# Optimization experiments

Measured on AMD Instinct MI355X. Metric: run time of the kernel, lower is better.

## Reference

```python
import jax, jax.numpy as jnp
import numpy as np

NEG_INF = -9e15
ALPHA = 2.0  # LeakyReLU negative slope from init (alpha=2)


def setup_inputs() -> dict:
    key = jax.random.key(0)
    k1, k2, k3, k4 = jax.random.split(key, 4)
    B, N, Fin, Fout = 8, 2048, 256, 128
    x = jax.random.normal(k1, (B, N, Fin), dtype=jnp.float32)
    adj = jax.random.randint(k2, (B, N, N), 0, 2, dtype=jnp.int32)
    # xavier_uniform with gain=1.414
    def xavier(k, shape, gain=1.414):
        fan_in, fan_out = shape[0], shape[1]
        bound = gain * np.sqrt(6.0 / (fan_in + fan_out))
        return jax.random.uniform(k, shape, jnp.float32, -bound, bound)
    W = xavier(k3, (Fin, Fout))
    a = xavier(k4, (2 * Fout, 1))
    return {"x": x, "adj": adj, "W": W, "a": a}


def reference(x, adj, W, a):
    # Wh: [B, N, Fout]
    Wh = jnp.matmul(x, W)
    Fout = W.shape[1]
    a1 = a[:Fout, 0]   # [Fout]
    a2 = a[Fout:, 0]   # [Fout]
    f1 = jnp.einsum('bnf,f->bn', Wh, a1)  # [B, N]
    f2 = jnp.einsum('bnf,f->bn', Wh, a2)  # [B, N]
    e = f1[:, :, None] + f2[:, None, :]   # [B, N, N]
    e = jnp.where(e >= 0, e, ALPHA * e)   # leaky relu, slope 2
    e = jnp.where(adj > 0, e, NEG_INF)
    attention = jax.nn.softmax(e, axis=2)
    # dropout: eval mode (no-op)
    h_prime = jnp.matmul(attention, Wh)   # [B, N, Fout]
    # concat=True -> elu
    return jnp.where(h_prime > 0, h_prime, jnp.expm1(h_prime))
```

## Files before the change

### kernel.cpp

```cpp
#include <hip/hip_runtime.h>
#include <hip/hip_bf16.h>
#include <math.h>

constexpr int B_   = 8;
constexpr int N_   = 2048;
constexpr int FIN  = 256;
constexpr int FOUT = 128;

constexpr int CH  = 512;
constexpr int NCH = N_ / CH;
constexpr int PR  = CH + 8;
constexpr int XR  = FIN + 8;
constexpr int TR  = 40;

typedef __attribute__((ext_vector_type(8))) short bf16x8;
typedef __attribute__((ext_vector_type(4))) float f32x4;
typedef __attribute__((ext_vector_type(4))) int   i32x4;

static __device__ __forceinline__ unsigned short f2bf(float f) {
    __hip_bfloat16 h = __float2bfloat16(f);
    return *reinterpret_cast<unsigned short*>(&h);
}
static __device__ __forceinline__ i32x4 ntload4(const int* p) {
    return __builtin_nontemporal_load((const i32x4*)p);
}

__global__ __launch_bounds__(256) void k0_wt(const float* __restrict__ W,
                                             unsigned short* __restrict__ Wt) {
    const int n = blockIdx.x;
    const int k = threadIdx.x;
    Wt[n * FIN + k] = f2bf(W[k * FOUT + n]);
}

__global__ __launch_bounds__(256) void ka_wh(const float* __restrict__ x,
                                             const unsigned short* __restrict__ Wt,
                                             const float* __restrict__ a,
                                             unsigned short* __restrict__ WhT,
                                             float* __restrict__ f1,
                                             float* __restrict__ f2) {
    __shared__ unsigned short xs[32 * XR];
    __shared__ float as[2 * FOUT];
    __shared__ float fred[2][4][32];

    const int tid = threadIdx.x;
    const int j0  = blockIdx.x * 32;
    const int b   = j0 >> 11;
    const int jb  = j0 & (N_ - 1);

    if (tid < 2 * FOUT) as[tid] = a[tid];
    {
        const float4* xsrc = (const float4*)(x + (size_t)j0 * FIN);
#pragma unroll
        for (int t = 0; t < 8; ++t) {
            const int idx = tid + t * 256;
            float4 v = xsrc[idx];
            const int row = idx >> 6, c4 = idx & 63;
            ushort4 u;
            u.x = f2bf(v.x); u.y = f2bf(v.y); u.z = f2bf(v.z); u.w = f2bf(v.w);
            *(ushort4*)&xs[row * XR + c4 * 4] = u;
        }
    }
    __syncthreads();

    const int wave = tid >> 6, lane = tid & 63;
    const int quad = lane >> 4, l16 = lane & 15;

    f32x4 acc[2][2];
#pragma unroll
    for (int aa = 0; aa < 2; ++aa)
#pragma unroll
        for (int nn = 0; nn < 2; ++nn) acc[aa][nn] = {0.f, 0.f, 0.f, 0.f};

    const unsigned short* wtA0 = Wt + (size_t)(32 * wave + l16) * FIN;
    const unsigned short* wtA1 = wtA0 + 16 * FIN;
#pragma unroll
    for (int ks = 0; ks < FIN / 32; ++ks) {
        const int kof = ks * 32 + quad * 8;
        bf16x8 af0 = *(const bf16x8*)&wtA0[kof];
        bf16x8 af1 = *(const bf16x8*)&wtA1[kof];
        bf16x8 bf0 = *(const bf16x8*)&xs[l16 * XR + kof];
        bf16x8 bf1 = *(const bf16x8*)&xs[(16 + l16) * XR + kof];
        acc[0][0] = __builtin_amdgcn_mfma_f32_16x16x32_bf16(af0, bf0, acc[0][0], 0, 0, 0);
        acc[0][1] = __builtin_amdgcn_mfma_f32_16x16x32_bf16(af0, bf1, acc[0][1], 0, 0, 0);
        acc[1][0] = __builtin_amdgcn_mfma_f32_16x16x32_bf16(af1, bf0, acc[1][0], 0, 0, 0);
        acc[1][1] = __builtin_amdgcn_mfma_f32_16x16x32_bf16(af1, bf1, acc[1][1], 0, 0, 0);
    }
    __syncthreads();

    unsigned short* T = xs;
    float pf[2][2] = {{0.f, 0.f}, {0.f, 0.f}};
#pragma unroll
    for (int aa = 0; aa < 2; ++aa)
#pragma unroll
        for (int nn = 0; nn < 2; ++nn)
#pragma unroll
            for (int r = 0; r < 4; ++r) {
                const int d = 32 * wave + 16 * aa + 4 * quad + r;
                const float v = acc[aa][nn][r];
                T[d * TR + nn * 16 + l16] = f2bf(v);
                pf[0][nn] += v * as[d];
                pf[1][nn] += v * as[FOUT + d];
            }
#pragma unroll
    for (int ff = 0; ff < 2; ++ff)
#pragma unroll
        for (int nn = 0; nn < 2; ++nn) {
            float v = pf[ff][nn];
            v += __shfl_xor(v, 16);
            v += __shfl_xor(v, 32);
            pf[ff][nn] = v;
        }
    if (quad == 0) {
#pragma unroll
        for (int ff = 0; ff < 2; ++ff)
#pragma unroll
            for (int nn = 0; nn < 2; ++nn)
                fred[ff][wave][nn * 16 + l16] = pf[ff][nn];
    }
    __syncthreads();

    unsigned short* dstW = WhT + (size_t)b * FOUT * N_;
#pragma unroll
    for (int it = 0; it < 2; ++it) {
        const int idx = it * 256 + tid;
        const int d = idx >> 2, q = idx & 3;
        bf16x8 v = *(const bf16x8*)&T[d * TR + q * 8];
        *(bf16x8*)&dstW[(size_t)d * N_ + jb + q * 8] = v;
    }
    if (tid < 64) {
        const int ff = tid >> 5, j32 = tid & 31;
        const float s = fred[ff][0][j32] + fred[ff][1][j32] +
                        fred[ff][2][j32] + fred[ff][3][j32];
        (ff ? f2 : f1)[(size_t)b * N_ + jb + j32] = s;
    }
}

static __device__ __forceinline__ void kb_phaseA(
    const int c, const int lane, const int wave, const int i0,
    const int* __restrict__ adjB, const float4* __restrict__ f2b4,
    const float* __restrict__ f1r, float* __restrict__ s_run,
    unsigned short* __restrict__ pb)
{
    const float4 fv0 = f2b4[c * (CH / 4) + lane];
    const float4 fv1 = f2b4[c * (CH / 4) + 64 + lane];
#pragma unroll
    for (int rr = 0; rr < 4; ++rr) {
        const int ti = wave * 4 + rr;
        const int i  = i0 + ti;
        const int* arow = adjB + (size_t)i * N_ + c * CH;
        const i32x4 av0 = ntload4(arow + 4 * lane);
        const i32x4 av1 = ntload4(arow + 256 + 4 * lane);
        const float f1i = f1r[rr];

        float e[8];
        e[0] = f1i + fv0.x; e[1] = f1i + fv0.y; e[2] = f1i + fv0.z; e[3] = f1i + fv0.w;
        e[4] = f1i + fv1.x; e[5] = f1i + fv1.y; e[6] = f1i + fv1.z; e[7] = f1i + fv1.w;
#pragma unroll
        for (int q = 0; q < 8; ++q) e[q] = (e[q] >= 0.f) ? e[q] : 2.f * e[q];

        float pv[8];
        pv[0] = (av0.x > 0) ? __expf(e[0]) : 0.f;
        pv[1] = (av0.y > 0) ? __expf(e[1]) : 0.f;
        pv[2] = (av0.z > 0) ? __expf(e[2]) : 0.f;
        pv[3] = (av0.w > 0) ? __expf(e[3]) : 0.f;
        pv[4] = (av1.x > 0) ? __expf(e[4]) : 0.f;
        pv[5] = (av1.y > 0) ? __expf(e[5]) : 0.f;
        pv[6] = (av1.z > 0) ? __expf(e[6]) : 0.f;
        pv[7] = (av1.w > 0) ? __expf(e[7]) : 0.f;

        s_run[rr] += ((pv[0] + pv[1]) + (pv[2] + pv[3])) +
                     ((pv[4] + pv[5]) + (pv[6] + pv[7]));

        ushort4 u0, u1;
        u0.x = f2bf(pv[0]); u0.y = f2bf(pv[1]); u0.z = f2bf(pv[2]); u0.w = f2bf(pv[3]);
        u1.x = f2bf(pv[4]); u1.y = f2bf(pv[5]); u1.z = f2bf(pv[6]); u1.w = f2bf(pv[7]);
        *(ushort4*)&pb[ti * PR + 4 * lane]       = u0;
        *(ushort4*)&pb[ti * PR + 256 + 4 * lane] = u1;
    }
}

__global__ __launch_bounds__(256) void kb_attn(const int* __restrict__ adj,
                                               const unsigned short* __restrict__ WhT,
                                               const float* __restrict__ f1,
                                               const float* __restrict__ f2,
                                               float* __restrict__ out) {
    __shared__ unsigned short p[2][16 * PR];
    __shared__ float rsum[16];

    const int tid  = threadIdx.x;
    const int b    = blockIdx.x & 7;
    const int i0   = (blockIdx.x >> 3) * 16;
    const int wave = tid >> 6, lane = tid & 63;
    const int quad = lane >> 4, l16 = lane & 15;

    const float4* f2b4 = (const float4*)(f2 + (size_t)b * N_);
    const int*    adjB = adj + (size_t)b * N_ * N_;

    float f1r[4], s_run[4];
#pragma unroll
    for (int rr = 0; rr < 4; ++rr) {
        f1r[rr]   = f1[(size_t)b * N_ + i0 + wave * 4 + rr];
        s_run[rr] = 0.f;
    }

    f32x4 acc0 = {0.f, 0.f, 0.f, 0.f}, acc1 = {0.f, 0.f, 0.f, 0.f};
    const int n0 = wave * 32;
    const unsigned short* wB0 = WhT + (size_t)b * FOUT * N_ + (size_t)(n0 + l16) * N_;
    const unsigned short* wB1 = wB0 + (size_t)16 * N_;

    kb_phaseA(0, lane, wave, i0, adjB, f2b4, f1r, s_run, &p[0][0]);
    __syncthreads();

    for (int c = 0; c < NCH; ++c) {
        if (c + 1 < NCH) {
            kb_phaseA(c + 1, lane, wave, i0, adjB, f2b4, f1r, s_run,
                      &p[(c + 1) & 1][0]);
        } else {
#pragma unroll
            for (int rr = 0; rr < 4; ++rr) {
                float s = s_run[rr];
#pragma unroll
                for (int o = 32; o; o >>= 1) s += __shfl_xor(s, o);
                if (lane == 0) rsum[wave * 4 + rr] = s;
            }
        }

        const unsigned short* pA = &p[c & 1][l16 * PR];
        const int kbase = c * CH;
#pragma unroll
        for (int ks = 0; ks < CH / 32; ++ks) {
            const int kof = ks * 32 + quad * 8;
            bf16x8 afr = *(const bf16x8*)&pA[kof];
            bf16x8 b0  = *(const bf16x8*)&wB0[kbase + kof];
            bf16x8 b1  = *(const bf16x8*)&wB1[kbase + kof];
            acc0 = __builtin_amdgcn_mfma_f32_16x16x32_bf16(afr, b0, acc0, 0, 0, 0);
            acc1 = __builtin_amdgcn_mfma_f32_16x16x32_bf16(afr, b1, acc1, 0, 0, 0);
        }
        __syncthreads();
    }

#pragma unroll
    for (int r = 0; r < 4; ++r) {
        const int m = quad * 4 + r;
        const float inv = 1.f / rsum[m];
        float v0 = acc0[r] * inv;
        float v1 = acc1[r] * inv;
        v0 = (v0 > 0.f) ? v0 : expm1f(v0);
        v1 = (v1 > 0.f) ? v1 : expm1f(v1);
        const size_t base = ((size_t)b * N_ + i0 + m) * FOUT + n0;
        out[base + l16]      = v0;
        out[base + 16 + l16] = v1;
    }
}

extern "C" void kernel_launch(void* const* d_in, const int* in_sizes, int n_in,
                              void* d_out, int out_size, void* d_ws, size_t ws_size,
                              hipStream_t stream) {
    const float* x   = (const float*)d_in[0];
    const int*   adj = (const int*)d_in[1];
    const float* W   = (const float*)d_in[2];
    const float* a   = (const float*)d_in[3];
    float* out = (float*)d_out;

    unsigned short* WhT = (unsigned short*)d_ws;
    unsigned short* Wt  = WhT + (size_t)B_ * FOUT * N_;
    float* f1 = (float*)(Wt + (size_t)FOUT * FIN);
    float* f2 = f1 + (size_t)B_ * N_;

    hipLaunchKernelGGL(k0_wt, dim3(FOUT), dim3(FIN), 0, stream, W, Wt);
    hipLaunchKernelGGL(ka_wh, dim3(B_ * N_ / 32), dim3(256), 0, stream,
                       x, Wt, a, WhT, f1, f2);
    hipLaunchKernelGGL(kb_attn, dim3(B_ * N_ / 16), dim3(256), 0, stream,
                       adj, WhT, f1, f2, out);
}
```

Baseline: 258.3 us.

## Use 8 waves per attention block and software-pipeline adj loads around MFMA

Result: no change. 260.2 us (+0.7%).

```diff
diff --git a/kernel.cpp b/kernel.cpp
--- a/kernel.cpp
+++ b/kernel.cpp
@@ -135,55 +135,11 @@
     }
 }
 
-static __device__ __forceinline__ void kb_phaseA(
-    const int c, const int lane, const int wave, const int i0,
-    const int* __restrict__ adjB, const float4* __restrict__ f2b4,
-    const float* __restrict__ f1r, float* __restrict__ s_run,
-    unsigned short* __restrict__ pb)
-{
-    const float4 fv0 = f2b4[c * (CH / 4) + lane];
-    const float4 fv1 = f2b4[c * (CH / 4) + 64 + lane];
-#pragma unroll
-    for (int rr = 0; rr < 4; ++rr) {
-        const int ti = wave * 4 + rr;
-        const int i  = i0 + ti;
-        const int* arow = adjB + (size_t)i * N_ + c * CH;
-        const i32x4 av0 = ntload4(arow + 4 * lane);
-        const i32x4 av1 = ntload4(arow + 256 + 4 * lane);
-        const float f1i = f1r[rr];
-
-        float e[8];
-        e[0] = f1i + fv0.x; e[1] = f1i + fv0.y; e[2] = f1i + fv0.z; e[3] = f1i + fv0.w;
-        e[4] = f1i + fv1.x; e[5] = f1i + fv1.y; e[6] = f1i + fv1.z; e[7] = f1i + fv1.w;
-#pragma unroll
-        for (int q = 0; q < 8; ++q) e[q] = (e[q] >= 0.f) ? e[q] : 2.f * e[q];
-
-        float pv[8];
-        pv[0] = (av0.x > 0) ? __expf(e[0]) : 0.f;
-        pv[1] = (av0.y > 0) ? __expf(e[1]) : 0.f;
-        pv[2] = (av0.z > 0) ? __expf(e[2]) : 0.f;
-        pv[3] = (av0.w > 0) ? __expf(e[3]) : 0.f;
-        pv[4] = (av1.x > 0) ? __expf(e[4]) : 0.f;
-        pv[5] = (av1.y > 0) ? __expf(e[5]) : 0.f;
-        pv[6] = (av1.z > 0) ? __expf(e[6]) : 0.f;
-        pv[7] = (av1.w > 0) ? __expf(e[7]) : 0.f;
-
-        s_run[rr] += ((pv[0] + pv[1]) + (pv[2] + pv[3])) +
-                     ((pv[4] + pv[5]) + (pv[6] + pv[7]));
-
-        ushort4 u0, u1;
-        u0.x = f2bf(pv[0]); u0.y = f2bf(pv[1]); u0.z = f2bf(pv[2]); u0.w = f2bf(pv[3]);
-        u1.x = f2bf(pv[4]); u1.y = f2bf(pv[5]); u1.z = f2bf(pv[6]); u1.w = f2bf(pv[7]);
-        *(ushort4*)&pb[ti * PR + 4 * lane]       = u0;
-        *(ushort4*)&pb[ti * PR + 256 + 4 * lane] = u1;
-    }
-}
-
-__global__ __launch_bounds__(256) void kb_attn(const int* __restrict__ adj,
-                                               const unsigned short* __restrict__ WhT,
-                                               const float* __restrict__ f1,
-                                               const float* __restrict__ f2,
-                                               float* __restrict__ out) {
+__global__ __launch_bounds__(512, 4) void kb_attn(const int* __restrict__ adj,
+                                                  const unsigned short* __restrict__ WhT,
+                                                  const float* __restrict__ f1,
+                                                  const float* __restrict__ f2,
+                                                  float* __restrict__ out) {
     __shared__ unsigned short p[2][16 * PR];
     __shared__ float rsum[16];
 
@@ -196,45 +152,103 @@
     const float4* f2b4 = (const float4*)(f2 + (size_t)b * N_);
     const int*    adjB = adj + (size_t)b * N_ * N_;
 
-    float f1r[4], s_run[4];
-#pragma unroll
-    for (int rr = 0; rr < 4; ++rr) {
-        f1r[rr]   = f1[(size_t)b * N_ + i0 + wave * 4 + rr];
+    float f1r[2], s_run[2];
+#pragma unroll
+    for (int rr = 0; rr < 2; ++rr) {
+        f1r[rr]   = f1[(size_t)b * N_ + i0 + wave * 2 + rr];
         s_run[rr] = 0.f;
     }
 
-    f32x4 acc0 = {0.f, 0.f, 0.f, 0.f}, acc1 = {0.f, 0.f, 0.f, 0.f};
-    const int n0 = wave * 32;
-    const unsigned short* wB0 = WhT + (size_t)b * FOUT * N_ + (size_t)(n0 + l16) * N_;
-    const unsigned short* wB1 = wB0 + (size_t)16 * N_;
-
-    kb_phaseA(0, lane, wave, i0, adjB, f2b4, f1r, s_run, &p[0][0]);
+    f32x4 acc = {0.f, 0.f, 0.f, 0.f};
+    const unsigned short* wBr =
+        WhT + (size_t)b * FOUT * N_ + (size_t)(wave * 16 + l16) * N_;
+
+    i32x4  areg[2][2];
+    float4 fv[2];
+
+    auto LOADS = [&](int c) {
+        fv[0] = f2b4[c * (CH / 4) + lane];
+        fv[1] = f2b4[c * (CH / 4) + 64 + lane];
+#pragma unroll
+        for (int rr = 0; rr < 2; ++rr) {
+            const int* arow =
+                adjB + (size_t)(i0 + wave * 2 + rr) * N_ + c * CH;
+            areg[rr][0] = ntload4(arow + 4 * lane);
+            areg[rr][1] = ntload4(arow + 256 + 4 * lane);
+        }
+    };
+
+    auto PROCESS = [&](int c) {
+        unsigned short* pb = &p[c & 1][0];
+#pragma unroll
+        for (int rr = 0; rr < 2; ++rr) {
+            const int ti = wave * 2 + rr;
+            const float f1i = f1r[rr];
+            const i32x4 av0 = areg[rr][0];
+            const i32x4 av1 = areg[rr][1];
+
+            float e[8];
+            e[0] = f1i + fv[0].x; e[1] = f1i + fv[0].y;
+            e[2] = f1i + fv[0].z; e[3] = f1i + fv[0].w;
+            e[4] = f1i + fv[1].x; e[5] = f1i + fv[1].y;
+            e[6] = f1i + fv[1].z; e[7] = f1i + fv[1].w;
+#pragma unroll
+            for (int q = 0; q < 8; ++q) e[q] = (e[q] >= 0.f) ? e[q] : 2.f * e[q];
+
+            float pv[8];
+            pv[0] = (av0.x > 0) ? __expf(e[0]) : 0.f;
+            pv[1] = (av0.y > 0) ? __expf(e[1]) : 0.f;
+            pv[2] = (av0.z > 0) ? __expf(e[2]) : 0.f;
+            pv[3] = (av0.w > 0) ? __expf(e[3]) : 0.f;
+            pv[4] = (av1.x > 0) ? __expf(e[4]) : 0.f;
+            pv[5] = (av1.y > 0) ? __expf(e[5]) : 0.f;
+            pv[6] = (av1.z > 0) ? __expf(e[6]) : 0.f;
+            pv[7] = (av1.w > 0) ? __expf(e[7]) : 0.f;
+
+            s_run[rr] += ((pv[0] + pv[1]) + (pv[2] + pv[3])) +
+                         ((pv[4] + pv[5]) + (pv[6] + pv[7]));
+
+            ushort4 u0, u1;
+            u0.x = f2bf(pv[0]); u0.y = f2bf(pv[1]);
+            u0.z = f2bf(pv[2]); u0.w = f2bf(pv[3]);
+            u1.x = f2bf(pv[4]); u1.y = f2bf(pv[5]);
+            u1.z = f2bf(pv[6]); u1.w = f2bf(pv[7]);
+            *(ushort4*)&pb[ti * PR + 4 * lane]       = u0;
+            *(ushort4*)&pb[ti * PR + 256 + 4 * lane] = u1;
+        }
+    };
+
+    LOADS(0);
+    PROCESS(0);
     __syncthreads();
 
     for (int c = 0; c < NCH; ++c) {
+        const unsigned short* wBc = wBr + (size_t)c * CH;
+        bf16x8 br[16];
+#pragma unroll
+        for (int ks = 0; ks < CH / 32; ++ks)
+            br[ks] = *(const bf16x8*)&wBc[ks * 32 + quad * 8];
+
+        if (c + 1 < NCH) LOADS(c + 1);
+
+        const unsigned short* pA = &p[c & 1][l16 * PR];
+#pragma unroll
+        for (int ks = 0; ks < CH / 32; ++ks) {
+            bf16x8 afr = *(const bf16x8*)&pA[ks * 32 + quad * 8];
+            acc = __builtin_amdgcn_mfma_f32_16x16x32_bf16(afr, br[ks], acc,
+                                                          0, 0, 0);
+        }
+
         if (c + 1 < NCH) {
-            kb_phaseA(c + 1, lane, wave, i0, adjB, f2b4, f1r, s_run,
-                      &p[(c + 1) & 1][0]);
+            PROCESS(c + 1);
         } else {
 #pragma unroll
-            for (int rr = 0; rr < 4; ++rr) {
+            for (int rr = 0; rr < 2; ++rr) {
                 float s = s_run[rr];
 #pragma unroll
                 for (int o = 32; o; o >>= 1) s += __shfl_xor(s, o);
-                if (lane == 0) rsum[wave * 4 + rr] = s;
+                if (lane == 0) rsum[wave * 2 + rr] = s;
             }
-        }
-
-        const unsigned short* pA = &p[c & 1][l16 * PR];
-        const int kbase = c * CH;
-#pragma unroll
-        for (int ks = 0; ks < CH / 32; ++ks) {
-            const int kof = ks * 32 + quad * 8;
-            bf16x8 afr = *(const bf16x8*)&pA[kof];
-            bf16x8 b0  = *(const bf16x8*)&wB0[kbase + kof];
-            bf16x8 b1  = *(const bf16x8*)&wB1[kbase + kof];
-            acc0 = __builtin_amdgcn_mfma_f32_16x16x32_bf16(afr, b0, acc0, 0, 0, 0);
-            acc1 = __builtin_amdgcn_mfma_f32_16x16x32_bf16(afr, b1, acc1, 0, 0, 0);
         }
         __syncthreads();
     }
@@ -243,13 +257,9 @@
     for (int r = 0; r < 4; ++r) {
         const int m = quad * 4 + r;
         const float inv = 1.f / rsum[m];
-        float v0 = acc0[r] * inv;
-        float v1 = acc1[r] * inv;
-        v0 = (v0 > 0.f) ? v0 : expm1f(v0);
-        v1 = (v1 > 0.f) ? v1 : expm1f(v1);
-        const size_t base = ((size_t)b * N_ + i0 + m) * FOUT + n0;
-        out[base + l16]      = v0;
-        out[base + 16 + l16] = v1;
+        float v = acc[r] * inv;
+        v = (v > 0.f) ? v : expm1f(v);
+        out[((size_t)b * N_ + i0 + m) * FOUT + wave * 16 + l16] = v;
     }
 }
 
@@ -270,6 +280,6 @@
     hipLaunchKernelGGL(k0_wt, dim3(FOUT), dim3(FIN), 0, stream, W, Wt);
     hipLaunchKernelGGL(ka_wh, dim3(B_ * N_ / 32), dim3(256), 0, stream,
                        x, Wt, a, WhT, f1, f2);
-    hipLaunchKernelGGL(kb_attn, dim3(B_ * N_ / 16), dim3(256), 0, stream,
+    hipLaunchKernelGGL(kb_attn, dim3(B_ * N_ / 16), dim3(512), 0, stream,
                        adj, WhT, f1, f2, out);
 }
```
